# Kernel tuning notes

Hardware: AMD Instinct MI355X
Metric: run time of the kernel (lower is better)

## Reference

```python
import jax, jax.numpy as jnp
import numpy as np

VOCAB = 100000
SHORTLIST = 10000  # cutoffs = [10000, 20000, 40000, 80000], n_clusters = 4
B, T, D = 1024, 128, 1024


def setup_inputs() -> dict:
    key = jax.random.key(0)
    ks = jax.random.split(key, 12)
    s = 0.02  # realistic init scale for weights
    inp = {
        "features": jax.random.normal(ks[0], (B, D), jnp.float32),
        "head_weight": jax.random.normal(ks[1], (SHORTLIST + 4, D), jnp.float32) * s,
        "proj0": jax.random.normal(ks[2], (512, D), jnp.float32) * s,
        "out0": jax.random.normal(ks[3], (10000, 512), jnp.float32) * s,
        "proj1": jax.random.normal(ks[4], (256, D), jnp.float32) * s,
        "out1": jax.random.normal(ks[5], (20000, 256), jnp.float32) * s,
        "proj2": jax.random.normal(ks[6], (128, D), jnp.float32) * s,
        "out2": jax.random.normal(ks[7], (40000, 128), jnp.float32) * s,
        "proj3": jax.random.normal(ks[8], (64, D), jnp.float32) * s,
        "out3": jax.random.normal(ks[9], (20000, 64), jnp.float32) * s,
        "discard_probs": jax.random.uniform(ks[10], (VOCAB,), jnp.float32),
        "targets": jax.random.randint(ks[11], (B, T), 0, VOCAB, jnp.int64),
        "target_mask": jnp.ones((B, T), jnp.bool_),
    }
    return inp


def _adaptive_log_prob(x, head_weight, projs, outs):
    # head: shortlist logits + one logit per tail cluster
    head_lp = jax.nn.log_softmax(x @ head_weight.T, axis=-1)  # [B, SHORTLIST+4]
    parts = [head_lp[:, :SHORTLIST]]
    for i, (pw, ow) in enumerate(zip(projs, outs)):
        cluster_logits = (x @ pw.T) @ ow.T  # [B, osz]
        parts.append(jax.nn.log_softmax(cluster_logits, axis=-1)
                     + head_lp[:, SHORTLIST + i:SHORTLIST + i + 1])
    return jnp.concatenate(parts, axis=-1)  # [B, VOCAB]


def reference(features, head_weight, proj0, out0, proj1, out1, proj2, out2,
              proj3, out3, discard_probs, targets, target_mask):
    # dropout is identity in eval/reference mode
    logprob = _adaptive_log_prob(features, head_weight,
                                 (proj0, proj1, proj2, proj3),
                                 (out0, out1, out2, out3))
    lp_t = jnp.take_along_axis(logprob, targets, axis=1)        # [B, T]
    w = (1.0 - discard_probs[targets]) * target_mask.astype(lp_t.dtype)
    per_sample = jnp.sum(-lp_t * w, axis=1) / jnp.sum(w, axis=1)  # [B]
    return jnp.sum(per_sample) / (targets.shape[0] + 1e-5)
```

## Files before the change

### kernel.cpp

```cpp
#include <hip/hip_runtime.h>
#include <cstdint>


typedef unsigned short u16;
typedef __attribute__((ext_vector_type(4))) float f32x4;
typedef __attribute__((ext_vector_type(8))) __bf16 bf16x8;
typedef __attribute__((ext_vector_type(4))) unsigned int u32x4;

__device__ __forceinline__ u16 f2bf(float f){
  unsigned u = __float_as_uint(f);
  u += 0x7FFFu + ((u >> 16) & 1u);
  return (u16)(u >> 16);
}

__device__ __forceinline__ float wave_sum(float v){
  #pragma unroll
  for (int d = 1; d < 64; d <<= 1) v += __shfl_xor(v, d, 64);
  return v;
}

__device__ __forceinline__ void gload_lds16(const void* g, void* l){
  __builtin_amdgcn_global_load_lds(
      (const __attribute__((address_space(1))) unsigned int*)g,
      (__attribute__((address_space(3))) unsigned int*)l, 16, 0, 0);
}

struct CvtSeg { const float* src; u16* dst; unsigned start; };
struct CvtTab { CvtSeg s[10]; unsigned total; };

__global__ __launch_bounds__(256) void cvt_bf16(CvtTab t){
  unsigned stride = gridDim.x * blockDim.x;
  for (unsigned c = blockIdx.x*blockDim.x + threadIdx.x; c < t.total; c += stride){
    int si = 0;
    #pragma unroll
    for (int i = 1; i < 10; i++) if (c >= t.s[i].start) si = i;
    unsigned lo = c - t.s[si].start;
    const float4* sp = (const float4*)t.s[si].src + (size_t)lo*2;
    float4 f0 = sp[0], f1 = sp[1];
    uint4 d;
    d.x = (unsigned)f2bf(f0.x) | ((unsigned)f2bf(f0.y) << 16);
    d.y = (unsigned)f2bf(f0.z) | ((unsigned)f2bf(f0.w) << 16);
    d.z = (unsigned)f2bf(f1.x) | ((unsigned)f2bf(f1.y) << 16);
    d.w = (unsigned)f2bf(f1.z) | ((unsigned)f2bf(f1.w) << 16);
    ((uint4*)t.s[si].dst)[lo] = d;
  }
}

struct GSeg { const u16* A; const u16* B; float* part; u16* C; float* gates;
              int lda, N, K, ntiles, tileStart, ldc; };
struct GTab { GSeg seg[5]; int nseg; int swz; };

__global__ __launch_bounds__(256, 4) void gemm_all(GTab tab){
  __shared__ __attribute__((aligned(16))) u16 ldsA[128*64];
  __shared__ __attribute__((aligned(16))) u16 ldsB[128*64];
  __shared__ float msLds[128][2];

  int bx = blockIdx.x, by = blockIdx.y;
  if (tab.swz){
    int flat = by * 8 + bx;
    int xcd = flat & 7, j = flat >> 3;
    by = (j >> 3) * 8 + xcd;
    bx = j & 7;
    if (by >= (int)gridDim.y){ by = j; bx = xcd; }
  }

  int s = 0;
  #pragma unroll
  for (int i = 1; i < 5; i++)
    if (i < tab.nseg && by >= tab.seg[i].tileStart) s = i;
  const u16* Ab = tab.seg[s].A;
  const u16* Bb = tab.seg[s].B;
  float* part   = tab.seg[s].part;
  u16* Cc       = tab.seg[s].C;
  float* gatesp = tab.seg[s].gates;
  int lda = tab.seg[s].lda, N = tab.seg[s].N, K = tab.seg[s].K;
  int ldc = tab.seg[s].ldc;
  int tileN = by - tab.seg[s].tileStart;
  int n0 = tileN * 128;
  int row0 = bx * 128;

  int tid = threadIdx.x;
  int wid = tid >> 6, lane = tid & 63;
  int wr = wid >> 1, wc = wid & 1;
  int qr = lane >> 4, ln = lane & 15;

  const char* baseA = (const char*)(Ab + (size_t)row0*lda);
  const char* baseB = (const char*)Bb;
  unsigned offA[4], offB[4];
  #pragma unroll
  for (int t = 0; t < 4; t++){
    int c = t*256 + tid, row = c >> 3, jj = (c & 7) ^ (row & 7);
    offA[t] = (unsigned)(row*lda + jj*8) * 2u;
    int nr = n0 + row; if (nr >= N) nr = N - 1;
    offB[t] = (unsigned)(nr*K + jj*8) * 2u;
  }

  f32x4 acc[4][4];
  const f32x4 zero = {0.f, 0.f, 0.f, 0.f};
  #pragma unroll
  for (int i = 0; i < 4; i++)
    #pragma unroll
    for (int j = 0; j < 4; j++) acc[i][j] = zero;

  int nkt = K >> 6;
  for (int kt = 0; kt < nkt; kt++){
    __syncthreads();
    unsigned kb = (unsigned)kt * 128u;
    #pragma unroll
    for (int t = 0; t < 4; t++){
      gload_lds16(baseA + offA[t] + kb, (char*)ldsA + (size_t)(t*256 + tid)*16);
      gload_lds16(baseB + offB[t] + kb, (char*)ldsB + (size_t)(t*256 + tid)*16);
    }
    __syncthreads();
    #pragma unroll
    for (int ks = 0; ks < 2; ks++){
      bf16x8 av[4], bv[4];
      #pragma unroll
      for (int mt = 0; mt < 4; mt++){
        int rl = wr*64 + mt*16 + ln;
        int ch = rl*8 + ((ks*4 + qr) ^ (rl & 7));
        av[mt] = *(const bf16x8*)((const char*)ldsA + ch*16);
      }
      #pragma unroll
      for (int nt = 0; nt < 4; nt++){
        int rl = wc*64 + nt*16 + ln;
        int ch = rl*8 + ((ks*4 + qr) ^ (rl & 7));
        bv[nt] = *(const bf16x8*)((const char*)ldsB + ch*16);
      }
      #pragma unroll
      for (int mt = 0; mt < 4; mt++)
        #pragma unroll
        for (int nt = 0; nt < 4; nt++)
          acc[mt][nt] = __builtin_amdgcn_mfma_f32_16x16x32_bf16(av[mt], bv[nt], acc[mt][nt], 0, 0, 0);
    }
  }

  if (part){
    #pragma unroll
    for (int mt = 0; mt < 4; mt++){
      #pragma unroll
      for (int r = 0; r < 4; r++){
        float ss = 0.f;
        #pragma unroll
        for (int nt = 0; nt < 4; nt++){
          int col = n0 + wc*64 + nt*16 + ln;
          if (col < N){
            float v = acc[mt][nt][r];
            ss += __expf(v);
            if (gatesp && col >= 10000){
              int row = row0 + wr*64 + mt*16 + qr*4 + r;
              gatesp[row*4 + (col - 10000)] = v;
            }
          }
        }
        ss += __shfl_xor(ss, 1, 64);
        ss += __shfl_xor(ss, 2, 64);
        ss += __shfl_xor(ss, 4, 64);
        ss += __shfl_xor(ss, 8, 64);
        if (ln == 0) msLds[wr*64 + mt*16 + qr*4 + r][wc] = ss;
      }
    }
    __syncthreads();
    if (tid < 128)
      part[(size_t)(row0 + tid)*ldc + tileN] = msLds[tid][0] + msLds[tid][1];
  } else {
    #pragma unroll
    for (int mt = 0; mt < 4; mt++)
      #pragma unroll
      for (int nt = 0; nt < 4; nt++)
        #pragma unroll
        for (int r = 0; r < 4; r++){
          int col = n0 + wc*64 + nt*16 + ln;
          if (col < N){
            int row = row0 + wr*64 + mt*16 + qr*4 + r;
            Cc[(size_t)row*ldc + col] = f2bf(acc[mt][nt][r]);
          }
        }
  }
}

__device__ __forceinline__ float dot8pair(u32x4 va, u32x4 vb){
  float p = 0.f;
  #pragma unroll
  for (int i = 0; i < 4; i++){
    unsigned ua = va[i], ub = vb[i];
    p = fmaf(__uint_as_float(ua << 16),         __uint_as_float(ub << 16),         p);
    p = fmaf(__uint_as_float(ua & 0xFFFF0000u), __uint_as_float(ub & 0xFFFF0000u), p);
  }
  return p;
}

template<int T>
__device__ __forceinline__ float dotT(const u16* a, const u16* b, int gl){
  float s = 0.f;
  #pragma unroll
  for (int it = 0; it < T; it++){
    int k = gl*8 + it*128;
    s += dot8pair(*(const u32x4*)(a + k), *(const u32x4*)(b + k));
  }
  return s;
}

__device__ __forceinline__ float dot1m(const u16* a, const u16* b, int gl){
  int k = gl*8;
  int kc = k < 64 ? k : 0;
  float p = dot8pair(*(const u32x4*)(a + kc), *(const u32x4*)(b + kc));
  return k < 64 ? p : 0.f;
}

struct GatherArgs {
  const u16* Xb; const u16* Hb; const u16* Hact; const u16* Ob;
  const float* part; const float* gates; const int* targets;
  const float* discard; float* psamp;
};

__global__ __launch_bounds__(256) void gather_rows(GatherArgs g){
  __shared__ __attribute__((aligned(16))) u16 xr[1024];
  __shared__ __attribute__((aligned(16))) u16 hr[960];
  __shared__ __attribute__((aligned(16))) int tg[128];
  __shared__ int tgs[128];
  __shared__ int cntW[2][5];
  __shared__ float sLse[4][5];
  __shared__ float ls[5], gs[4];
  __shared__ float lpv[128];
  __shared__ float sa[2], sw[2];

  int b = blockIdx.x;
  int tid = threadIdx.x;
  int w = tid >> 6, lane = tid & 63;
  int grp = tid >> 4, gl = tid & 15;

  if (tid < 128) ((u32x4*)xr)[tid] = ((const u32x4*)(g.Xb + (size_t)b*1024))[tid];
  else if (tid < 248) ((u32x4*)hr)[tid-128] = ((const u32x4*)(g.Hact + (size_t)b*960))[tid-128];
  if (tid < 32) ((u32x4*)tg)[tid] = ((const u32x4*)(g.targets + (size_t)b*128))[tid];
  if (tid < 4) gs[tid] = g.gates[b*4 + tid];

  {
    const float* pr = g.part + (size_t)b*785;
    float p0=0.f, p1=0.f, p2=0.f, p3=0.f, p4=0.f;
    for (int j = tid; j < 785; j += 256){
      float v = pr[j];
      if      (j <  79) p0 += v;
      else if (j < 158) p1 += v;
      else if (j < 315) p2 += v;
      else if (j < 628) p3 += v;
      else              p4 += v;
    }
    p0 = wave_sum(p0); p1 = wave_sum(p1); p2 = wave_sum(p2);
    p3 = wave_sum(p3); p4 = wave_sum(p4);
    if (lane == 0){
      sLse[w][0]=p0; sLse[w][1]=p1; sLse[w][2]=p2; sLse[w][3]=p3; sLse[w][4]=p4;
    }
  }
  __syncthreads();
  if (tid < 5)
    ls[tid] = __logf(sLse[0][tid] + sLse[1][tid] + sLse[2][tid] + sLse[3][tid]);

  int vb128 = tg[tid & 127];
  int bkt = (vb128 >= 10000) + (vb128 >= 20000) + (vb128 >= 40000) + (vb128 >= 80000);
  unsigned long long ltm = (1ULL << lane) - 1ULL;
  int rank = 0;
  #pragma unroll
  for (int c = 0; c < 5; c++){
    unsigned long long m = __ballot(bkt == c);
    if (bkt == c) rank = __popcll(m & ltm);
    if (lane == 0 && w < 2) cntW[w][c] = (int)__popcll(m);
  }
  __syncthreads();
  if (tid < 128){
    int base = 0;
    #pragma unroll
    for (int c = 0; c < 5; c++)
      base += (c < bkt) ? (cntW[0][c] + cntW[1][c]) : 0;
    int pos = base + (w == 1 ? cntW[0][bkt] : 0) + rank;
    tgs[pos] = vb128;
  }
  __syncthreads();

  for (int t = 0; t < 8; t++){
    int ti = t*16 + grp;
    int v = tgs[ti];
    bool head = v < 10000;
    int c = (v >= 20000) + (v >= 40000) + (v >= 80000);
    float s;
    if (head)       s = dotT<8>(xr,       g.Hb + (size_t)v*1024, gl);
    else if (c==0)  s = dotT<4>(hr,       g.Ob + (size_t)(v-10000)*512, gl);
    else if (c==1)  s = dotT<2>(hr + 512, g.Ob + 5120000u  + (size_t)(v-20000)*256, gl);
    else if (c==2)  s = dotT<1>(hr + 768, g.Ob + 10240000u + (size_t)(v-40000)*128, gl);
    else            s = dot1m  (hr + 896, g.Ob + 15360000u + (size_t)(v-80000)*64,  gl);
    s += __shfl_xor(s, 1, 64);
    s += __shfl_xor(s, 2, 64);
    s += __shfl_xor(s, 4, 64);
    s += __shfl_xor(s, 8, 64);
    float bias = head ? -ls[0] : (gs[c] - ls[0] - ls[c + 1]);
    if (gl == 0) lpv[ti] = s + bias;
  }
  __syncthreads();

  if (tid < 128){
    int v = tgs[tid];
    float wt = 1.0f - g.discard[v];
    float a  = -lpv[tid] * wt;
    float as = wave_sum(a), ws = wave_sum(wt);
    if (lane == 0){ sa[w] = as; sw[w] = ws; }
  }
  __syncthreads();
  if (tid == 0) g.psamp[b] = (sa[0] + sa[1]) / (sw[0] + sw[1]);
}

__global__ __launch_bounds__(256) void final_sum(const float* psamp, float* out){
  float s = 0.f;
  for (int i = threadIdx.x; i < 1024; i += 256) s += psamp[i];
  s = wave_sum(s);
  __shared__ float sb[4];
  if ((threadIdx.x & 63) == 0) sb[threadIdx.x >> 6] = s;
  __syncthreads();
  if (threadIdx.x == 0) out[0] = (sb[0] + sb[1] + sb[2] + sb[3]) / (1024.0f + 1e-5f);
}

extern "C" void kernel_launch(void* const* d_in, const int* in_sizes, int n_in,
                              void* d_out, int out_size, void* d_ws, size_t ws_size,
                              hipStream_t stream){
  (void)in_sizes; (void)n_in; (void)out_size; (void)ws_size;
  const float* features = (const float*)d_in[0];
  const float* head_w   = (const float*)d_in[1];
  const float* proj[4]  = {(const float*)d_in[2], (const float*)d_in[4],
                           (const float*)d_in[6], (const float*)d_in[8]};
  const float* outw[4]  = {(const float*)d_in[3], (const float*)d_in[5],
                           (const float*)d_in[7], (const float*)d_in[9]};
  const float* discard  = (const float*)d_in[10];
  const int*   targets  = (const int*)d_in[11];
  float* out = (float*)d_out;

  char* wsp = (char*)d_ws;
  size_t off = 0;
  auto carve = [&](size_t bytes)->char*{
    char* p = wsp + off; off += (bytes + 255) & ~(size_t)255; return p;
  };
  u16* Xb     = (u16*)carve(1024ull*1024*2);
  u16* Hb     = (u16*)carve(10004ull*1024*2);
  u16* Pb     = (u16*)carve(960ull*1024*2);
  u16* Ob     = (u16*)carve(16640000ull*2);
  u16* Hact   = (u16*)carve(1024ull*960*2);
  float* part = (float*)carve(803840ull*4);
  float* gates= (float*)carve(4096*4);
  float* psamp= (float*)carve(1024*4);

  CvtTab ct{};
  const float* srcs[10] = {features, head_w, proj[0], proj[1], proj[2], proj[3],
                           outw[0], outw[1], outw[2], outw[3]};
  u16* dsts[10] = {Xb, Hb, Pb, Pb + 512*1024, Pb + 768*1024, Pb + 896*1024,
                   Ob, Ob + 5120000, Ob + 10240000, Ob + 15360000};
  unsigned counts[10] = {1048576u, 10244096u, 524288u, 262144u, 131072u, 65536u,
                         5120000u, 5120000u, 5120000u, 1280000u};
  unsigned pre = 0;
  for (int i = 0; i < 10; i++){
    ct.s[i].src = srcs[i]; ct.s[i].dst = dsts[i]; ct.s[i].start = pre;
    pre += counts[i] / 8;
  }
  ct.total = pre;
  cvt_bf16<<<dim3(4096), dim3(256), 0, stream>>>(ct);

  GTab tp{};
  tp.nseg = 4; tp.swz = 0;
  tp.seg[0] = {Xb, Pb,            nullptr, Hact,       nullptr, 1024, 512, 1024, 4, 0, 960};
  tp.seg[1] = {Xb, Pb + 512*1024, nullptr, Hact + 512, nullptr, 1024, 256, 1024, 2, 4, 960};
  tp.seg[2] = {Xb, Pb + 768*1024, nullptr, Hact + 768, nullptr, 1024, 128, 1024, 1, 6, 960};
  tp.seg[3] = {Xb, Pb + 896*1024, nullptr, Hact + 896, nullptr, 1024, 64,  1024, 1, 7, 960};
  gemm_all<<<dim3(8, 8), dim3(256), 0, stream>>>(tp);

  GTab tm{};
  tm.nseg = 5; tm.swz = 1;
  tm.seg[0] = {Xb,         Hb,            part,       nullptr, gates,   1024, 10004, 1024, 79,  0,   785};
  tm.seg[1] = {Hact,       Ob,            part + 79,  nullptr, nullptr, 960,  10000, 512,  79,  79,  785};
  tm.seg[2] = {Hact + 512, Ob + 5120000,  part + 158, nullptr, nullptr, 960,  20000, 256,  157, 158, 785};
  tm.seg[3] = {Hact + 768, Ob + 10240000, part + 315, nullptr, nullptr, 960,  40000, 128,  313, 315, 785};
  tm.seg[4] = {Hact + 896, Ob + 15360000, part + 628, nullptr, nullptr, 960,  20000, 64,   157, 628, 785};
  gemm_all<<<dim3(8, 785), dim3(256), 0, stream>>>(tm);

  GatherArgs ga{Xb, Hb, Hact, Ob, part, gates, targets, discard, psamp};
  gather_rows<<<dim3(1024), dim3(256), 0, stream>>>(ga);

  final_sum<<<dim3(1), dim3(256), 0, stream>>>(psamp, out);
}
```

Before: 292.1 us.

## Fuse fp32-to-bf16 weight conversion into GEMM B-tile loads and gather

Removes the separate bulk conversion of all weight matrices (about 27M floats) to bf16. The GEMM now reads fp32 weight rows directly, converts them in registers, and writes bf16 into LDS. The gather kernel likewise reads fp32 weights. This drops a full write-then-read pass over the bf16 copies of the weights. In exchange, weight reads from global memory double in size, and the B-tile path goes through registers instead of an asynchronous direct-to-LDS load, which may add latency and register pressure in the main GEMM.

```diff
diff --git a/kernel.cpp b/kernel.cpp
--- a/kernel.cpp
+++ b/kernel.cpp
@@ -25,28 +25,21 @@
       (__attribute__((address_space(3))) unsigned int*)l, 16, 0, 0);
 }
 
-struct CvtSeg { const float* src; u16* dst; unsigned start; };
-struct CvtTab { CvtSeg s[10]; unsigned total; };
-
-__global__ __launch_bounds__(256) void cvt_bf16(CvtTab t){
-  unsigned stride = gridDim.x * blockDim.x;
-  for (unsigned c = blockIdx.x*blockDim.x + threadIdx.x; c < t.total; c += stride){
-    int si = 0;
-    #pragma unroll
-    for (int i = 1; i < 10; i++) if (c >= t.s[i].start) si = i;
-    unsigned lo = c - t.s[si].start;
-    const float4* sp = (const float4*)t.s[si].src + (size_t)lo*2;
+__global__ __launch_bounds__(256) void cvt_feat(const float* src, u16* dst, int nchunks){
+  int c = blockIdx.x*256 + threadIdx.x;
+  if (c < nchunks){
+    const float4* sp = (const float4*)src + (size_t)c*2;
     float4 f0 = sp[0], f1 = sp[1];
     uint4 d;
     d.x = (unsigned)f2bf(f0.x) | ((unsigned)f2bf(f0.y) << 16);
     d.y = (unsigned)f2bf(f0.z) | ((unsigned)f2bf(f0.w) << 16);
     d.z = (unsigned)f2bf(f1.x) | ((unsigned)f2bf(f1.y) << 16);
     d.w = (unsigned)f2bf(f1.z) | ((unsigned)f2bf(f1.w) << 16);
-    ((uint4*)t.s[si].dst)[lo] = d;
-  }
-}
-
-struct GSeg { const u16* A; const u16* B; float* part; u16* C; float* gates;
+    ((uint4*)dst)[c] = d;
+  }
+}
+
+struct GSeg { const u16* A; const float* B; float* part; u16* C; float* gates;
               int lda, N, K, ntiles, tileStart, ldc; };
 struct GTab { GSeg seg[5]; int nseg; int swz; };
 
@@ -68,8 +61,8 @@
   #pragma unroll
   for (int i = 1; i < 5; i++)
     if (i < tab.nseg && by >= tab.seg[i].tileStart) s = i;
-  const u16* Ab = tab.seg[s].A;
-  const u16* Bb = tab.seg[s].B;
+  const u16* Ab   = tab.seg[s].A;
+  const float* Bf = tab.seg[s].B;
   float* part   = tab.seg[s].part;
   u16* Cc       = tab.seg[s].C;
   float* gatesp = tab.seg[s].gates;
@@ -85,14 +78,13 @@
   int qr = lane >> 4, ln = lane & 15;
 
   const char* baseA = (const char*)(Ab + (size_t)row0*lda);
-  const char* baseB = (const char*)Bb;
-  unsigned offA[4], offB[4];
+  unsigned offA[4], offBe[4];
   #pragma unroll
   for (int t = 0; t < 4; t++){
     int c = t*256 + tid, row = c >> 3, jj = (c & 7) ^ (row & 7);
     offA[t] = (unsigned)(row*lda + jj*8) * 2u;
     int nr = n0 + row; if (nr >= N) nr = N - 1;
-    offB[t] = (unsigned)(nr*K + jj*8) * 2u;
+    offBe[t] = (unsigned)(nr*K + jj*8);
   }
 
   f32x4 acc[4][4];
@@ -105,11 +97,26 @@
   int nkt = K >> 6;
   for (int kt = 0; kt < nkt; kt++){
     __syncthreads();
-    unsigned kb = (unsigned)kt * 128u;
+    unsigned kbA = (unsigned)kt * 128u;
+    unsigned kbE = (unsigned)kt * 64u;
+    float4 b0[4], b1[4];
     #pragma unroll
     for (int t = 0; t < 4; t++){
-      gload_lds16(baseA + offA[t] + kb, (char*)ldsA + (size_t)(t*256 + tid)*16);
-      gload_lds16(baseB + offB[t] + kb, (char*)ldsB + (size_t)(t*256 + tid)*16);
+      const float* bp = Bf + offBe[t] + kbE;
+      b0[t] = *(const float4*)bp;
+      b1[t] = *(const float4*)(bp + 4);
+    }
+    #pragma unroll
+    for (int t = 0; t < 4; t++)
+      gload_lds16(baseA + offA[t] + kbA, (char*)ldsA + (size_t)(t*256 + tid)*16);
+    #pragma unroll
+    for (int t = 0; t < 4; t++){
+      bf16x8 w;
+      w[0] = (__bf16)b0[t].x; w[1] = (__bf16)b0[t].y;
+      w[2] = (__bf16)b0[t].z; w[3] = (__bf16)b0[t].w;
+      w[4] = (__bf16)b1[t].x; w[5] = (__bf16)b1[t].y;
+      w[6] = (__bf16)b1[t].z; w[7] = (__bf16)b1[t].w;
+      *(bf16x8*)((char*)ldsB + (size_t)(t*256 + tid)*16) = w;
     }
     __syncthreads();
     #pragma unroll
@@ -179,37 +186,40 @@
   }
 }
 
-__device__ __forceinline__ float dot8pair(u32x4 va, u32x4 vb){
+__device__ __forceinline__ float dotf8(u32x4 va, const float* wp){
+  float4 w0 = *(const float4*)wp, w1 = *(const float4*)(wp + 4);
+  float w[8] = {w0.x, w0.y, w0.z, w0.w, w1.x, w1.y, w1.z, w1.w};
   float p = 0.f;
   #pragma unroll
   for (int i = 0; i < 4; i++){
-    unsigned ua = va[i], ub = vb[i];
-    p = fmaf(__uint_as_float(ua << 16),         __uint_as_float(ub << 16),         p);
-    p = fmaf(__uint_as_float(ua & 0xFFFF0000u), __uint_as_float(ub & 0xFFFF0000u), p);
+    unsigned ua = va[i];
+    p = fmaf(__uint_as_float(ua << 16),         (float)(__bf16)w[2*i],     p);
+    p = fmaf(__uint_as_float(ua & 0xFFFF0000u), (float)(__bf16)w[2*i + 1], p);
   }
   return p;
 }
 
 template<int T>
-__device__ __forceinline__ float dotT(const u16* a, const u16* b, int gl){
+__device__ __forceinline__ float dotTf(const u16* a, const float* b, int gl){
   float s = 0.f;
   #pragma unroll
   for (int it = 0; it < T; it++){
     int k = gl*8 + it*128;
-    s += dot8pair(*(const u32x4*)(a + k), *(const u32x4*)(b + k));
+    s += dotf8(*(const u32x4*)(a + k), b + k);
   }
   return s;
 }
 
-__device__ __forceinline__ float dot1m(const u16* a, const u16* b, int gl){
+__device__ __forceinline__ float dot1mf(const u16* a, const float* b, int gl){
   int k = gl*8;
   int kc = k < 64 ? k : 0;
-  float p = dot8pair(*(const u32x4*)(a + kc), *(const u32x4*)(b + kc));
+  float p = dotf8(*(const u32x4*)(a + kc), b + kc);
   return k < 64 ? p : 0.f;
 }
 
 struct GatherArgs {
-  const u16* Xb; const u16* Hb; const u16* Hact; const u16* Ob;
+  const u16* Xb; const float* HbF; const u16* Hact;
+  const float* O0; const float* O1; const float* O2; const float* O3;
   const float* part; const float* gates; const int* targets;
   const float* discard; float* psamp;
 };
@@ -283,11 +293,11 @@
     bool head = v < 10000;
     int c = (v >= 20000) + (v >= 40000) + (v >= 80000);
     float s;
-    if (head)       s = dotT<8>(xr,       g.Hb + (size_t)v*1024, gl);
-    else if (c==0)  s = dotT<4>(hr,       g.Ob + (size_t)(v-10000)*512, gl);
-    else if (c==1)  s = dotT<2>(hr + 512, g.Ob + 5120000u  + (size_t)(v-20000)*256, gl);
-    else if (c==2)  s = dotT<1>(hr + 768, g.Ob + 10240000u + (size_t)(v-40000)*128, gl);
-    else            s = dot1m  (hr + 896, g.Ob + 15360000u + (size_t)(v-80000)*64,  gl);
+    if (head)       s = dotTf<8>(xr,       g.HbF + (size_t)v*1024, gl);
+    else if (c==0)  s = dotTf<4>(hr,       g.O0 + (size_t)(v-10000)*512, gl);
+    else if (c==1)  s = dotTf<2>(hr + 512, g.O1 + (size_t)(v-20000)*256, gl);
+    else if (c==2)  s = dotTf<1>(hr + 768, g.O2 + (size_t)(v-40000)*128, gl);
+    else            s = dot1mf (hr + 896,  g.O3 + (size_t)(v-80000)*64,  gl);
     s += __shfl_xor(s, 1, 64);
     s += __shfl_xor(s, 2, 64);
     s += __shfl_xor(s, 4, 64);
@@ -338,47 +348,32 @@
     char* p = wsp + off; off += (bytes + 255) & ~(size_t)255; return p;
   };
   u16* Xb     = (u16*)carve(1024ull*1024*2);
-  u16* Hb     = (u16*)carve(10004ull*1024*2);
-  u16* Pb     = (u16*)carve(960ull*1024*2);
-  u16* Ob     = (u16*)carve(16640000ull*2);
   u16* Hact   = (u16*)carve(1024ull*960*2);
   float* part = (float*)carve(803840ull*4);
   float* gates= (float*)carve(4096*4);
   float* psamp= (float*)carve(1024*4);
 
-  CvtTab ct{};
-  const float* srcs[10] = {features, head_w, proj[0], proj[1], proj[2], proj[3],
-                           outw[0], outw[1], outw[2], outw[3]};
-  u16* dsts[10] = {Xb, Hb, Pb, Pb + 512*1024, Pb + 768*1024, Pb + 896*1024,
-                   Ob, Ob + 5120000, Ob + 10240000, Ob + 15360000};
-  unsigned counts[10] = {1048576u, 10244096u, 524288u, 262144u, 131072u, 65536u,
-                         5120000u, 5120000u, 5120000u, 1280000u};
-  unsigned pre = 0;
-  for (int i = 0; i < 10; i++){
-    ct.s[i].src = srcs[i]; ct.s[i].dst = dsts[i]; ct.s[i].start = pre;
-    pre += counts[i] / 8;
-  }
-  ct.total = pre;
-  cvt_bf16<<<dim3(4096), dim3(256), 0, stream>>>(ct);
+  cvt_feat<<<dim3(512), dim3(256), 0, stream>>>(features, Xb, 131072);
 
   GTab tp{};
   tp.nseg = 4; tp.swz = 0;
-  tp.seg[0] = {Xb, Pb,            nullptr, Hact,       nullptr, 1024, 512, 1024, 4, 0, 960};
-  tp.seg[1] = {Xb, Pb + 512*1024, nullptr, Hact + 512, nullptr, 1024, 256, 1024, 2, 4, 960};
-  tp.seg[2] = {Xb, Pb + 768*1024, nullptr, Hact + 768, nullptr, 1024, 128, 1024, 1, 6, 960};
-  tp.seg[3] = {Xb, Pb + 896*1024, nullptr, Hact + 896, nullptr, 1024, 64,  1024, 1, 7, 960};
+  tp.seg[0] = {Xb, proj[0], nullptr, Hact,       nullptr, 1024, 512, 1024, 4, 0, 960};
+  tp.seg[1] = {Xb, proj[1], nullptr, Hact + 512, nullptr, 1024, 256, 1024, 2, 4, 960};
+  tp.seg[2] = {Xb, proj[2], nullptr, Hact + 768, nullptr, 1024, 128, 1024, 1, 6, 960};
+  tp.seg[3] = {Xb, proj[3], nullptr, Hact + 896, nullptr, 1024, 64,  1024, 1, 7, 960};
   gemm_all<<<dim3(8, 8), dim3(256), 0, stream>>>(tp);
 
   GTab tm{};
   tm.nseg = 5; tm.swz = 1;
-  tm.seg[0] = {Xb,         Hb,            part,       nullptr, gates,   1024, 10004, 1024, 79,  0,   785};
-  tm.seg[1] = {Hact,       Ob,            part + 79,  nullptr, nullptr, 960,  10000, 512,  79,  79,  785};
-  tm.seg[2] = {Hact + 512, Ob + 5120000,  part + 158, nullptr, nullptr, 960,  20000, 256,  157, 158, 785};
-  tm.seg[3] = {Hact + 768, Ob + 10240000, part + 315, nullptr, nullptr, 960,  40000, 128,  313, 315, 785};
-  tm.seg[4] = {Hact + 896, Ob + 15360000, part + 628, nullptr, nullptr, 960,  20000, 64,   157, 628, 785};
+  tm.seg[0] = {Xb,         head_w,  part,       nullptr, gates,   1024, 10004, 1024, 79,  0,   785};
+  tm.seg[1] = {Hact,       outw[0], part + 79,  nullptr, nullptr, 960,  10000, 512,  79,  79,  785};
+  tm.seg[2] = {Hact + 512, outw[1], part + 158, nullptr, nullptr, 960,  20000, 256,  157, 158, 785};
+  tm.seg[3] = {Hact + 768, outw[2], part + 315, nullptr, nullptr, 960,  40000, 128,  313, 315, 785};
+  tm.seg[4] = {Hact + 896, outw[3], part + 628, nullptr, nullptr, 960,  20000, 64,   157, 628, 785};
   gemm_all<<<dim3(8, 785), dim3(256), 0, stream>>>(tm);
 
-  GatherArgs ga{Xb, Hb, Hact, Ob, part, gates, targets, discard, psamp};
+  GatherArgs ga{Xb, head_w, Hact, outw[0], outw[1], outw[2], outw[3],
+                part, gates, targets, discard, psamp};
   gather_rows<<<dim3(1024), dim3(256), 0, stream>>>(ga);
 
   final_sum<<<dim3(1), dim3(256), 0, stream>>>(psamp, out);
```

Result: slower. 298.5 us (+2.2%).
